# Kernel tuning notes

Measured on AMD Instinct MI355X. Metric: run time of the kernel, lower is better.

Reference implementation:

```python
import jax, jax.numpy as jnp
import numpy as np
from jax import lax

N_RAYS, N_STEPS, G = 4096, 160, 160
COLOR_DIM, WIDTH = 3, 128
POS_PE, VIEW_PE = 5, 4
XYZ_MIN, XYZ_MAX = -1.0, 1.0
NEAR = 0.05
STEPSIZE = 0.5
VOXEL_SIZE = (XYZ_MAX - XYZ_MIN) / G
DIST = STEPSIZE * VOXEL_SIZE
S_VAL = 80.0
FASTCOLOR_THRES = 1e-7
MASK_THRES = 1e-3
ALPHA_INIT = 1e-4
ACT_SHIFT = float(np.log(1.0 / (1.0 - ALPHA_INIT) - 1.0))
SMOOTH_K, SMOOTH_SIGMA = 5, 1.0
POSFREQ = jnp.asarray([2.0 ** i for i in range(POS_PE)], jnp.float32)
VIEWFREQ = jnp.asarray([2.0 ** i for i in range(VIEW_PE)], jnp.float32)


def _gauss_kernel():
    ax = np.arange(SMOOTH_K) - SMOOTH_K // 2
    g = np.exp(-(ax ** 2) / (2.0 * SMOOTH_SIGMA ** 2))
    k = g[:, None, None] * g[None, :, None] * g[None, None, :]
    return jnp.asarray(k / k.sum(), np.float32)[None, None]


def _trilerp(grid, pts):
    # grid [C,Gx,Gx,Gx]; pts [...,3] in world coords -> [..., C] (align_corners trilinear)
    Gx = grid.shape[-1]
    u = (pts - XYZ_MIN) / (XYZ_MAX - XYZ_MIN) * (Gx - 1)
    u = jnp.clip(u, 0.0, Gx - 1.0)
    i0 = jnp.clip(jnp.floor(u).astype(jnp.int32), 0, Gx - 2)
    f = u - i0.astype(u.dtype)
    x0, y0, z0 = i0[..., 0], i0[..., 1], i0[..., 2]
    fx, fy, fz = f[..., 0], f[..., 1], f[..., 2]
    def g8(ix, iy, iz):
        return grid[:, ix, iy, iz]  # [C, ...]
    out = (g8(x0, y0, z0) * (1 - fx) * (1 - fy) * (1 - fz)
         + g8(x0, y0, z0 + 1) * (1 - fx) * (1 - fy) * fz
         + g8(x0, y0 + 1, z0) * (1 - fx) * fy * (1 - fz)
         + g8(x0, y0 + 1, z0 + 1) * (1 - fx) * fy * fz
         + g8(x0 + 1, y0, z0) * fx * (1 - fy) * (1 - fz)
         + g8(x0 + 1, y0, z0 + 1) * fx * (1 - fy) * fz
         + g8(x0 + 1, y0 + 1, z0) * fx * fy * (1 - fz)
         + g8(x0 + 1, y0 + 1, z0 + 1) * fx * fy * fz)
    return jnp.moveaxis(out, 0, -1)


def _alphas2weights(alpha):
    # per-ray (segmented) exclusive cumprod of transmittance; alpha [N,S]
    T = jnp.cumprod(1.0 - alpha, axis=1)
    T_excl = jnp.concatenate([jnp.ones_like(T[:, :1]), T[:, :-1]], axis=1)
    return alpha * T_excl, T[:, -1]


def _mlp(x, w0, b0, w1, b1, w2, b2):
    h = jax.nn.relu(x @ w0 + b0)
    h = jax.nn.relu(h @ w1 + b1)
    return h @ w2 + b2


def _forward(rays_o, rays_d, viewdirs, sdf_grid, mask_density,
             off_color_grid, emo_color_grid,
             off_w0, off_b0, off_w1, off_b1, off_w2, off_b2,
             emo_w0, emo_b0, emo_w1, emo_b1, emo_w2, emo_b2, em_modes):
    N = rays_o.shape[0]
    t = NEAR + DIST * jnp.arange(N_STEPS, dtype=jnp.float32)
    ray_pts = rays_o[:, None, :] + rays_d[:, None, :] * t[None, :, None]  # [N,S,3]

    # MaskCache: threshold alpha from coarse density grid (boolean keep mask)
    dens = _trilerp(mask_density, ray_pts)[..., 0]
    mask_alpha = 1.0 - jnp.exp(-jax.nn.softplus(dens + ACT_SHIFT) * DIST)
    keep0 = mask_alpha >= MASK_THRES  # [N,S]

    # Gaussian-smoothed SDF grid + central-difference gradient grid
    sdf_s = lax.conv_general_dilated(sdf_grid, _gauss_kernel(), (1, 1, 1), 'SAME',
                                     dimension_numbers=('NCDHW', 'OIDHW', 'NCDHW'))[0]  # [1,G,G,G]
    s = sdf_s[0]
    grad_grid = jnp.zeros((3, G, G, G), sdf_grid.dtype)
    grad_grid = grad_grid.at[0, 1:-1].set((s[2:] - s[:-2]) / (2 * VOXEL_SIZE))
    grad_grid = grad_grid.at[1, :, 1:-1].set((s[:, 2:] - s[:, :-2]) / (2 * VOXEL_SIZE))
    grad_grid = grad_grid.at[2, :, :, 1:-1].set((s[:, :, 2:] - s[:, :, :-2]) / (2 * VOXEL_SIZE))

    sdf = _trilerp(sdf_s, ray_pts)[..., 0]   # [N,S]
    gradient = _trilerp(grad_grid, ray_pts)  # [N,S,3]

    # NeuS alpha from sdf (scatter, grad variant, cos_anneal = 1)
    true_cos = jnp.einsum('nd,nsd->ns', viewdirs, gradient)
    iter_cos = -jax.nn.relu(-true_cos)
    prev_cdf = jax.nn.sigmoid((sdf - iter_cos * DIST * 0.5) * S_VAL)
    next_cdf = jax.nn.sigmoid((sdf + iter_cos * DIST * 0.5) * S_VAL)
    alpha = jnp.clip((prev_cdf - next_cdf + 1e-5) / (prev_cdf + 1e-5), 0.0, 1.0)
    alpha = jnp.where(keep0, alpha, 0.0)  # masked points contribute nothing

    weights, _ = _alphas2weights(alpha)
    keep1 = weights > FASTCOLOR_THRES
    alpha = jnp.where(keep1, alpha, 0.0)
    weights, alphainv_last = _alphas2weights(alpha)

    # features: pos PE, view PE (per-ray, gathered by ray_id == broadcast), normal
    rays_xyz = (ray_pts - XYZ_MIN) / (XYZ_MAX - XYZ_MIN)  # [N,S,3]
    xyz_emb = (rays_xyz[..., None] * POSFREQ).reshape(N, N_STEPS, -1)
    v_emb = (viewdirs[..., None] * VIEWFREQ).reshape(N, -1)
    v_full = jnp.concatenate([v_emb, jnp.sin(v_emb), jnp.cos(v_emb)], -1)
    v_full = jnp.broadcast_to(v_full[:, None, :], (N, N_STEPS, v_full.shape[-1]))
    normal = gradient / (jnp.linalg.norm(gradient, axis=-1, keepdims=True) + 1e-5)
    rgb_feat = jnp.concatenate([rays_xyz, jnp.sin(xyz_emb), jnp.cos(xyz_emb), v_full, normal], -1)

    off_in = jnp.concatenate([_trilerp(off_color_grid, ray_pts), rgb_feat], -1)
    emo_in = jnp.concatenate([_trilerp(emo_color_grid, ray_pts), rgb_feat], -1)
    off_rgb = jax.nn.sigmoid(_mlp(off_in, off_w0, off_b0, off_w1, off_b1, off_w2, off_b2))
    emo_rgb = jax.nn.sigmoid(_mlp(emo_in, emo_w0, emo_b0, emo_w1, emo_b1, emo_w2, emo_b2))
    on_mask = (em_modes == 1)[:, None, None]  # em_modes[ray_id] == 1
    rgb = jnp.where(on_mask, emo_rgb, 0.0) + off_rgb

    w_ = weights[..., None]
    rgb_marched = jnp.sum(w_ * rgb, axis=1)  # segment_coo(sum over ray_id)
    cum_weights = jnp.sum(w_, axis=1)        # [N,1]
    return rgb_marched, alphainv_last, 1.0 - cum_weights


def setup_inputs() -> dict:
    key = jax.random.key(0)
    ks = jax.random.split(key, 12)
    rays_o = jax.random.uniform(ks[0], (N_RAYS, 3), jnp.float32, -0.3, 0.3)
    rd = jax.random.normal(ks[1], (N_RAYS, 3), jnp.float32)
    rays_d = rd / jnp.linalg.norm(rd, axis=-1, keepdims=True)
    viewdirs = rays_d
    em_modes = jax.random.randint(ks[2], (N_RAYS,), 0, 2)
    lin = np.linspace(-1.0, 1.0, G, dtype=np.float32)
    x, y, z = np.meshgrid(lin, lin, lin, indexing='ij')
    sdf_grid = jnp.asarray(np.sqrt(x ** 2 + y ** 2 + z ** 2) - 1.0)[None, None]  # sphere-SDF init
    mask_density = jax.random.normal(ks[3], (1, 80, 80, 80), jnp.float32) * 2.0 + 12.0
    off_color_grid = jax.random.normal(ks[4], (COLOR_DIM, G, G, G), jnp.float32) * 0.1
    emo_color_grid = jax.random.normal(ks[5], (COLOR_DIM, G, G, G), jnp.float32) * 0.1
    DIM0 = 3 + 3 * POS_PE * 2 + 3 * VIEW_PE * 3 + COLOR_DIM + 3  # = 75
    def lw(k, i, o):
        return jax.random.normal(k, (i, o), jnp.float32) * (1.0 / np.sqrt(i))
    return dict(rays_o=rays_o, rays_d=rays_d, viewdirs=viewdirs, em_modes=em_modes,
                sdf_grid=sdf_grid, mask_density=mask_density,
                off_color_grid=off_color_grid, emo_color_grid=emo_color_grid,
                off_w0=lw(ks[6], DIM0, WIDTH), off_b0=jnp.zeros((WIDTH,), jnp.float32),
                off_w1=lw(ks[7], WIDTH, WIDTH), off_b1=jnp.zeros((WIDTH,), jnp.float32),
                off_w2=lw(ks[8], WIDTH, 3), off_b2=jnp.zeros((3,), jnp.float32),
                emo_w0=lw(ks[9], DIM0, WIDTH), emo_b0=jnp.zeros((WIDTH,), jnp.float32),
                emo_w1=lw(ks[10], WIDTH, WIDTH), emo_b1=jnp.zeros((WIDTH,), jnp.float32),
                emo_w2=lw(ks[11], WIDTH, 3), emo_b2=jnp.zeros((3,), jnp.float32))


def reference(rays_o, rays_d, viewdirs, em_modes, sdf_grid, mask_density,
              off_color_grid, emo_color_grid,
              off_w0, off_b0, off_w1, off_b1, off_w2, off_b2,
              emo_w0, emo_b0, emo_w1, emo_b1, emo_w2, emo_b2):
    return _forward(rays_o, rays_d, viewdirs, sdf_grid, mask_density,
                    off_color_grid, emo_color_grid,
                    off_w0, off_b0, off_w1, off_b1, off_w2, off_b2,
                    emo_w0, emo_b0, emo_w1, emo_b1, emo_w2, emo_b2, em_modes)
```

## Files before the change

### kernel.cpp

```cpp
#include <hip/hip_runtime.h>

#define NRAYS 4096
#define NSTEPS 160
#define NSAMP (NRAYS*NSTEPS)
#define GG 160
#define GG2 (GG*GG)
#define GG3 (GG*GG2)
#define GM 80
#define GM2 (GM*GM)

#define NEARV 0.05f
#define DISTV 0.00625f
#define SVAL 80.0f
#define ACT_SHIFT_C (-9.2102403669758813f)
#define INV2H 40.0f
#define MASK_THRES_C 1e-3f
#define FAST_THRES_C 1e-7f

#define KW0 0.05448868454964295f
#define KW1 0.24420134200323332f
#define KW2 0.40261994689424750f

__device__ __forceinline__ float sigmf(float x){ return 1.0f/(1.0f+__expf(-x)); }
__device__ __forceinline__ float softplusf_(float x){ return (x>20.0f)? x : log1pf(__expf(x)); }

__device__ __forceinline__ void tricoord(float p, int Gx, int& i0, float& fr){
  float u = (p + 1.0f)*0.5f*(float)(Gx-1);
  u = fminf(fmaxf(u, 0.0f), (float)(Gx-1));
  int i = (int)floorf(u);
  i = min(max(i,0), Gx-2);
  i0 = i; fr = u - (float)i;
}

__global__ __launch_bounds__(256) void ksmooth_yz(const float* __restrict__ in, float* __restrict__ out,
                                                  float* __restrict__ outbuf, int* __restrict__ cnt){
  __shared__ float S[36][37];
  __shared__ float Tz[36][33];
  const int bx = blockIdx.x;
  const int t = threadIdx.x;
  if (bx == 0){
    for (int i = t; i < NRAYS*3; i += 256) outbuf[i] = 0.0f;
    if (t == 0) *cnt = 0;
  }
  const int x  = bx / 25;
  const int tile = bx % 25;
  const int Y0 = (tile/5)*32, Z0 = (tile%5)*32;
  const float kw[5] = {KW0,KW1,KW2,KW1,KW0};
  for (int i = t; i < 36*36; i += 256){
    int r = i/36, c = i - (i/36)*36;
    int y = Y0 + r - 2, z = Z0 + c - 2;
    float v = 0.0f;
    if (y>=0 && y<GG && z>=0 && z<GG) v = in[(x*GG+y)*GG+z];
    S[r][c] = v;
  }
  __syncthreads();
  for (int i = t; i < 36*32; i += 256){
    int r = i >> 5, c = i & 31;
    float acc = 0.f;
    #pragma unroll
    for (int d=0; d<5; d++) acc += kw[d]*S[r][c+d];
    Tz[r][c] = acc;
  }
  __syncthreads();
  for (int i = t; i < 32*32; i += 256){
    int yy = i >> 5, c = i & 31;
    float acc = 0.f;
    #pragma unroll
    for (int d=0; d<5; d++) acc += kw[d]*Tz[yy+d][c];
    out[(x*GG + Y0+yy)*GG + Z0 + c] = acc;
  }
}

__global__ __launch_bounds__(64) void kmarch(
  const float* __restrict__ ro, const float* __restrict__ rd,
  const float* __restrict__ vd, const float* __restrict__ maskg,
  const float* __restrict__ Y,
  int* __restrict__ slist, float* __restrict__ sw, float* __restrict__ sgrad,
  int* __restrict__ cnt, float* __restrict__ out)
{
  int n = blockIdx.x*64 + threadIdx.x;
  if (n >= NRAYS) return;
  const float ox=ro[n*3+0], oy=ro[n*3+1], oz=ro[n*3+2];
  const float dx=rd[n*3+0], dy=rd[n*3+1], dz=rd[n*3+2];
  const float vx=vd[n*3+0], vy=vd[n*3+1], vz=vd[n*3+2];
  const float kwc[5] = {KW0,KW1,KW2,KW1,KW0};
  float T1=1.0f, T2=1.0f, cum=0.0f;
  for (int s=0; s<NSTEPS; s++){
    float tt = NEARV + DISTV*(float)s;
    float px = ox + dx*tt, py = oy + dy*tt, pz = oz + dz*tt;

    int mx,my,mz; float mfx,mfy,mfz;
    tricoord(px, GM, mx, mfx); tricoord(py, GM, my, mfy); tricoord(pz, GM, mz, mfz);
    int mid = (mx*GM + my)*GM + mz;
    float d000=maskg[mid],        d001=maskg[mid+1];
    float d010=maskg[mid+GM],     d011=maskg[mid+GM+1];
    float d100=maskg[mid+GM2],    d101=maskg[mid+GM2+1];
    float d110=maskg[mid+GM2+GM], d111=maskg[mid+GM2+GM+1];
    float m00 = d000 + (d001-d000)*mfz;
    float m01 = d010 + (d011-d010)*mfz;
    float m10 = d100 + (d101-d100)*mfz;
    float m11 = d110 + (d111-d110)*mfz;
    float m0 = m00 + (m01-m00)*mfy;
    float m1 = m10 + (m11-m10)*mfy;
    float dens = m0 + (m1-m0)*mfx;
    float malpha = 1.0f - __expf(-softplusf_(dens + ACT_SHIFT_C)*DISTV);

    int ix,iy,iz; float fx,fy,fz;
    tricoord(px, GG, ix, fx); tricoord(py, GG, iy, fy); tricoord(pz, GG, iz, fz);

    float R[2][2][8];
    #pragma unroll
    for (int jb=0;jb<2;jb++)
      #pragma unroll
      for (int jc=0;jc<2;jc++)
        #pragma unroll
        for (int j=0;j<8;j++){
          int a = ix-3+j;
          R[jb][jc][j] = (a>=0 && a<GG) ? Y[(a*GG + iy+jb)*GG + iz+jc] : 0.0f;
        }
    const bool hasym = (iy>=1), hasyp = (iy<=GG-3);
    const bool haszm = (iz>=1), haszp = (iz<=GG-3);
    float Eym[2][6], Eyp[2][6], Ezm[2][6], Ezp[2][6];
    #pragma unroll
    for (int jc=0;jc<2;jc++)
      #pragma unroll
      for (int j=0;j<6;j++){
        int a = ix-2+j;
        bool ax = (a>=0 && a<GG);
        Eym[jc][j] = (hasym && ax) ? Y[(a*GG + iy-1)*GG + iz+jc] : 0.0f;
        Eyp[jc][j] = (hasyp && ax) ? Y[(a*GG + iy+2)*GG + iz+jc] : 0.0f;
      }
    #pragma unroll
    for (int jb=0;jb<2;jb++)
      #pragma unroll
      for (int j=0;j<6;j++){
        int a = ix-2+j;
        bool ax = (a>=0 && a<GG);
        Ezm[jb][j] = (haszm && ax) ? Y[(a*GG + iy+jb)*GG + iz-1] : 0.0f;
        Ezp[jb][j] = (haszp && ax) ? Y[(a*GG + iy+jb)*GG + iz+2] : 0.0f;
      }

    float sdf=0.0f, gx=0.0f, gy=0.0f, gz=0.0f;
    #pragma unroll
    for (int ja=0;ja<2;ja++){
      #pragma unroll
      for (int jb=0;jb<2;jb++){
        #pragma unroll
        for (int jc=0;jc<2;jc++){
          float w = (ja?fx:1.0f-fx)*(jb?fy:1.0f-fy)*(jc?fz:1.0f-fz);
          const float* r = R[jb][jc];
          float s0=0.0f;
          #pragma unroll
          for (int t2=0;t2<5;t2++) s0 += kwc[t2]*r[ja+1+t2];
          sdf += w*s0;
          int a = ix+ja, b = iy+jb, c = iz+jc;
          if (a>=1 && a<=GG-2){
            float sp=0.0f, sm=0.0f;
            #pragma unroll
            for (int t2=0;t2<5;t2++){ sp += kwc[t2]*r[ja+2+t2]; sm += kwc[t2]*r[ja+t2]; }
            gx += w*INV2H*(sp-sm);
          }
          if (b>=1 && b<=GG-2){
            float acc=0.0f;
            if (jb==0){
              const float* up = R[1][jc];
              const float* dn = Eym[jc];
              #pragma unroll
              for (int t2=0;t2<5;t2++) acc += kwc[t2]*(up[ja+1+t2] - dn[ja+t2]);
            } else {
              const float* up = Eyp[jc];
              const float* dn = R[0][jc];
              #pragma unroll
              for (int t2=0;t2<5;t2++) acc += kwc[t2]*(up[ja+t2] - dn[ja+1+t2]);
            }
            gy += w*INV2H*acc;
          }
          if (c>=1 && c<=GG-2){
            float acc=0.0f;
            if (jc==0){
              const float* up = R[jb][1];
              const float* dn = Ezm[jb];
              #pragma unroll
              for (int t2=0;t2<5;t2++) acc += kwc[t2]*(up[ja+1+t2] - dn[ja+t2]);
            } else {
              const float* up = Ezp[jb];
              const float* dn = R[jb][0];
              #pragma unroll
              for (int t2=0;t2<5;t2++) acc += kwc[t2]*(up[ja+t2] - dn[ja+1+t2]);
            }
            gz += w*INV2H*acc;
          }
        }
      }
    }

    float tc = vx*gx + vy*gy + vz*gz;
    float icos = fminf(tc, 0.0f);
    float e = icos*DISTV*0.5f;
    float prev = sigmf((sdf - e)*SVAL);
    float nxt  = sigmf((sdf + e)*SVAL);
    float alpha = (prev - nxt + 1e-5f)/(prev + 1e-5f);
    alpha = fminf(fmaxf(alpha, 0.0f), 1.0f);
    if (!(malpha >= MASK_THRES_C)) alpha = 0.0f;

    float w1 = alpha*T1; T1 *= (1.0f - alpha);
    float a2 = (w1 > FAST_THRES_C) ? alpha : 0.0f;
    float wv = a2*T2;   T2 *= (1.0f - a2);
    cum += wv;
    if (wv > 0.0f){
      int pos = atomicAdd(cnt, 1);
      slist[pos] = n*NSTEPS + s;
      sw[pos] = wv;
      sgrad[pos*3+0]=gx; sgrad[pos*3+1]=gy; sgrad[pos*3+2]=gz;
    }
    if (T1 <= FAST_THRES_C) break;
  }
  out[NRAYS*3 + n] = T2;
  out[NRAYS*4 + n] = 1.0f - cum;
}

__global__ __launch_bounds__(256) void kmlp3(
  const float* __restrict__ ro, const float* __restrict__ rd,
  const float* __restrict__ vd, const int* __restrict__ em,
  const float* __restrict__ offc, const float* __restrict__ emoc,
  const int* __restrict__ slist, const float* __restrict__ sw,
  const float* __restrict__ sgrad, const int* __restrict__ cnt,
  const float* __restrict__ W0o, const float* __restrict__ b0o,
  const float* __restrict__ W1o, const float* __restrict__ b1o,
  const float* __restrict__ W2o, const float* __restrict__ b2o,
  const float* __restrict__ W0e, const float* __restrict__ b0e,
  const float* __restrict__ W1e, const float* __restrict__ b1e,
  const float* __restrict__ W2e, const float* __restrict__ b2e,
  float* __restrict__ out)
{
  __shared__ float X[8][80];
  __shared__ float H[8][132];
  __shared__ float H2[8][132];
  __shared__ float OUTB[8][3];
  __shared__ float WSH[8];
  __shared__ float GS[8][3];
  __shared__ int SSAMP[8];
  __shared__ int SEM[8];
  __shared__ int s_go;

  const int t = threadIdx.x;
  const int count = *cnt;
  const int head = blockIdx.x & 1;
  const int cstride = gridDim.x >> 1;

  const float* W0 = head ? W0e : W0o;  const float* b0 = head ? b0e : b0o;
  const float* W1 = head ? W1e : W1o;  const float* b1 = head ? b1e : b1o;
  const float* W2 = head ? W2e : W2o;  const float* b2 = head ? b2e : b2o;
  const float* cg = head ? emoc : offc;
  const float4* W04 = (const float4*)W0;
  const float4* W14 = (const float4*)W1;

  const int sp   = t >> 5;
  const int lane = t & 31;

  for (int chunk = blockIdx.x >> 1; chunk*8 < count; chunk += cstride) {
    const int base = chunk*8;
    if (t == 0) s_go = 0;
    if (t < 8) {
      int i = base + t;
      bool vld = (i < count);
      int samp = vld ? slist[i] : 0;
      SSAMP[t] = samp;
      WSH[t]   = vld ? sw[i] : 0.0f;
      GS[t][0] = vld ? sgrad[i*3+0] : 0.0f;
      GS[t][1] = vld ? sgrad[i*3+1] : 0.0f;
      GS[t][2] = vld ? sgrad[i*3+2] : 0.0f;
      SEM[t]   = vld ? em[samp/NSTEPS] : 0;
    }
    __syncthreads();
    if (t < 8) {
      bool live = (WSH[t] > 0.0f) && (head == 0 || SEM[t] != 0);
      if (live) s_go = 1;
    }
    __syncthreads();

    if (s_go) {
      {
        const int s = t & 7;
        const int r = t >> 3;
        const int samp = SSAMP[s];
        const int n = samp / NSTEPS;
        const int step = samp - n*NSTEPS;
        const float tt = NEARV + DISTV*(float)step;
        const float px = ro[n*3+0] + rd[n*3+0]*tt;
        const float py = ro[n*3+1] + rd[n*3+1]*tt;
        const float pz = ro[n*3+2] + rd[n*3+2]*tt;
        if (r < 3) {
          int ix,iy,iz; float fx,fy,fz;
          tricoord(px, GG, ix, fx); tricoord(py, GG, iy, fy); tricoord(pz, GG, iz, fz);
          const float* g = cg + (size_t)r * GG3;
          const int id = (ix*GG + iy)*GG + iz;
          float v000=g[id],        v001=g[id+1];
          float v010=g[id+GG],     v011=g[id+GG+1];
          float v100=g[id+GG2],    v101=g[id+GG2+1];
          float v110=g[id+GG2+GG], v111=g[id+GG2+GG+1];
          float c00 = v000 + (v001-v000)*fz;
          float c01 = v010 + (v011-v010)*fz;
          float c10 = v100 + (v101-v100)*fz;
          float c11 = v110 + (v111-v110)*fz;
          float c0 = c00 + (c01-c00)*fy;
          float c1 = c10 + (c11-c10)*fy;
          X[s][r] = c0 + (c1-c0)*fx;
        } else if (r == 3) {
          X[s][3] = (px+1.0f)*0.5f;
          X[s][4] = (py+1.0f)*0.5f;
          X[s][5] = (pz+1.0f)*0.5f;
          float gx = GS[s][0], gy = GS[s][1], gz = GS[s][2];
          float inv = 1.0f/(sqrtf(gx*gx+gy*gy+gz*gz)+1e-5f);
          X[s][72] = gx*inv; X[s][73] = gy*inv; X[s][74] = gz*inv;
        } else if (r < 7) {
          const int a = r - 4;
          const float coord = (a==0)?px:((a==1)?py:pz);
          const float rxyz = (coord+1.0f)*0.5f;
          float fr = 1.0f;
          #pragma unroll
          for (int q = 0; q < 5; q++) {
            float e = rxyz*fr; fr *= 2.0f;
            X[s][6  + a*5 + q] = __sinf(e);
            X[s][21 + a*5 + q] = __cosf(e);
          }
        } else if (r < 10) {
          const int a = r - 7;
          const float v = vd[n*3+a];
          float fr = 1.0f;
          #pragma unroll
          for (int q = 0; q < 4; q++) {
            float e = v*fr; fr *= 2.0f;
            X[s][36 + a*4 + q] = e;
            X[s][48 + a*4 + q] = __sinf(e);
            X[s][60 + a*4 + q] = __cosf(e);
          }
        }
      }
      __syncthreads();

      {
        float4 acc = ((const float4*)b0)[lane];
        #pragma unroll 5
        for (int k=0; k<75; k++){
          float x = X[sp][k];
          float4 w = W04[k*32 + lane];
          acc.x += x*w.x; acc.y += x*w.y; acc.z += x*w.z; acc.w += x*w.w;
        }
        H[sp][lane*4+0] = fmaxf(acc.x,0.0f);
        H[sp][lane*4+1] = fmaxf(acc.y,0.0f);
        H[sp][lane*4+2] = fmaxf(acc.z,0.0f);
        H[sp][lane*4+3] = fmaxf(acc.w,0.0f);
      }
      __syncthreads();

      {
        float4 acc = ((const float4*)b1)[lane];
        #pragma unroll 8
        for (int k=0; k<128; k++){
          float x = H[sp][k];
          float4 w = W14[k*32 + lane];
          acc.x += x*w.x; acc.y += x*w.y; acc.z += x*w.z; acc.w += x*w.w;
        }
        H2[sp][lane*4+0] = fmaxf(acc.x,0.0f);
        H2[sp][lane*4+1] = fmaxf(acc.y,0.0f);
        H2[sp][lane*4+2] = fmaxf(acc.z,0.0f);
        H2[sp][lane*4+3] = fmaxf(acc.w,0.0f);
      }
      __syncthreads();

      {
        float a0=0.0f, a1=0.0f, a2v=0.0f;
        #pragma unroll
        for (int i=0;i<4;i++){
          int k = lane*4+i;
          float h = H2[sp][k];
          a0  += h*W2[k*3+0];
          a1  += h*W2[k*3+1];
          a2v += h*W2[k*3+2];
        }
        #pragma unroll
        for (int d=16; d>=1; d>>=1){
          a0  += __shfl_down(a0,  d, 32);
          a1  += __shfl_down(a1,  d, 32);
          a2v += __shfl_down(a2v, d, 32);
        }
        if (lane == 0){
          OUTB[sp][0] = sigmf(a0  + b2[0]);
          OUTB[sp][1] = sigmf(a1  + b2[1]);
          OUTB[sp][2] = sigmf(a2v + b2[2]);
        }
      }
      __syncthreads();

      if (t < 24) {
        int s2 = t/3, c = t - s2*3;
        float w = WSH[s2];
        if (w > 0.0f && (head == 0 || SEM[s2] != 0)) {
          int n2 = SSAMP[s2]/NSTEPS;
          atomicAdd(&out[n2*3 + c], w * OUTB[s2][c]);
        }
      }
    }
    __syncthreads();
  }
}

extern "C" void kernel_launch(void* const* d_in, const int* in_sizes, int n_in,
                              void* d_out, int out_size, void* d_ws, size_t ws_size,
                              hipStream_t stream) {
  const float* ro    = (const float*)d_in[0];
  const float* rd    = (const float*)d_in[1];
  const float* vd    = (const float*)d_in[2];
  const int*   em    = (const int*)d_in[3];
  const float* sdfg  = (const float*)d_in[4];
  const float* maskg = (const float*)d_in[5];
  const float* offc  = (const float*)d_in[6];
  const float* emoc  = (const float*)d_in[7];
  const float* W0o = (const float*)d_in[8];
  const float* b0o = (const float*)d_in[9];
  const float* W1o = (const float*)d_in[10];
  const float* b1o = (const float*)d_in[11];
  const float* W2o = (const float*)d_in[12];
  const float* b2o = (const float*)d_in[13];
  const float* W0e = (const float*)d_in[14];
  const float* b0e = (const float*)d_in[15];
  const float* W1e = (const float*)d_in[16];
  const float* b1e = (const float*)d_in[17];
  const float* W2e = (const float*)d_in[18];
  const float* b2e = (const float*)d_in[19];

  float* out = (float*)d_out;
  float* ws  = (float*)d_ws;
  float* bufB  = ws;
  float* swb   = ws + GG3;
  float* sgradb= swb + NSAMP;
  int*   slist = (int*)(sgradb + 3*(size_t)NSAMP);
  int*   cnt   = slist + NSAMP;

  ksmooth_yz<<<GG*25, 256, 0, stream>>>(sdfg, bufB, out, cnt);

  kmarch<<<NRAYS/64, 64, 0, stream>>>(ro, rd, vd, maskg, bufB,
                                      slist, swb, sgradb, cnt, out);

  kmlp3<<<2048, 256, 0, stream>>>(ro, rd, vd, em, offc, emoc,
                                  slist, swb, sgradb, cnt,
                                  W0o,b0o,W1o,b1o,W2o,b2o,
                                  W0e,b0e,W1e,b1e,W2e,b2e, out);
}
```

Measured before the change: 66.89 us.

## Register-block MLP over four samples per warp with 32-sample chunks

The MLP kernel now handles 32 samples per block instead of 8. Each 32-lane group computes four samples at once, so every weight float4 loaded from global memory is reused across four accumulators, and inputs are read from shared memory as float4. Feature-building work is spread over the 8 thread rows, with view encoding merged into the positional-encoding threads, and the grid is cut to 512 blocks. This is meant to cut the weight load traffic per sample, at the cost of more registers, more shared memory and fewer blocks to spread the work.

```diff
diff --git a/kernel.cpp b/kernel.cpp
--- a/kernel.cpp
+++ b/kernel.cpp
@@ -219,7 +219,7 @@
   out[NRAYS*4 + n] = 1.0f - cum;
 }
 
-__global__ __launch_bounds__(256) void kmlp3(
+__global__ __launch_bounds__(256) void kmlp5(
   const float* __restrict__ ro, const float* __restrict__ rd,
   const float* __restrict__ vd, const int* __restrict__ em,
   const float* __restrict__ offc, const float* __restrict__ emoc,
@@ -233,14 +233,14 @@
   const float* __restrict__ W2e, const float* __restrict__ b2e,
   float* __restrict__ out)
 {
-  __shared__ float X[8][80];
-  __shared__ float H[8][132];
-  __shared__ float H2[8][132];
-  __shared__ float OUTB[8][3];
-  __shared__ float WSH[8];
-  __shared__ float GS[8][3];
-  __shared__ int SSAMP[8];
-  __shared__ int SEM[8];
+  __shared__ float X[32][80];
+  __shared__ float H[32][132];
+  __shared__ float H2[32][132];
+  __shared__ float OUTB[32][3];
+  __shared__ float WSH[32];
+  __shared__ float GS[32][3];
+  __shared__ int SSAMP[32];
+  __shared__ int SEM[32];
   __shared__ int s_go;
 
   const int t = threadIdx.x;
@@ -255,13 +255,13 @@
   const float4* W04 = (const float4*)W0;
   const float4* W14 = (const float4*)W1;
 
-  const int sp   = t >> 5;
   const int lane = t & 31;
-
-  for (int chunk = blockIdx.x >> 1; chunk*8 < count; chunk += cstride) {
-    const int base = chunk*8;
+  const int sg   = t >> 5;
+
+  for (int chunk = blockIdx.x >> 1; chunk*32 < count; chunk += cstride) {
+    const int base = chunk*32;
     if (t == 0) s_go = 0;
-    if (t < 8) {
+    if (t < 32) {
       int i = base + t;
       bool vld = (i < count);
       int samp = vld ? slist[i] : 0;
@@ -273,7 +273,7 @@
       SEM[t]   = vld ? em[samp/NSTEPS] : 0;
     }
     __syncthreads();
-    if (t < 8) {
+    if (t < 32) {
       bool live = (WSH[t] > 0.0f) && (head == 0 || SEM[t] != 0);
       if (live) s_go = 1;
     }
@@ -281,8 +281,8 @@
 
     if (s_go) {
       {
-        const int s = t & 7;
-        const int r = t >> 3;
+        const int s = t & 31;
+        const int r = t >> 5;
         const int samp = SSAMP[s];
         const int n = samp / NSTEPS;
         const int step = samp - n*NSTEPS;
@@ -313,6 +313,7 @@
           float gx = GS[s][0], gy = GS[s][1], gz = GS[s][2];
           float inv = 1.0f/(sqrtf(gx*gx+gy*gy+gz*gz)+1e-5f);
           X[s][72] = gx*inv; X[s][73] = gy*inv; X[s][74] = gz*inv;
+          X[s][75] = 0.0f; X[s][76] = 0.0f; X[s][77] = 0.0f; X[s][78] = 0.0f; X[s][79] = 0.0f;
         } else if (r < 7) {
           const int a = r - 4;
           const float coord = (a==0)?px:((a==1)?py:pz);
@@ -324,13 +325,11 @@
             X[s][6  + a*5 + q] = __sinf(e);
             X[s][21 + a*5 + q] = __cosf(e);
           }
-        } else if (r < 10) {
-          const int a = r - 7;
           const float v = vd[n*3+a];
-          float fr = 1.0f;
+          float fr2 = 1.0f;
           #pragma unroll
           for (int q = 0; q < 4; q++) {
-            float e = v*fr; fr *= 2.0f;
+            float e = v*fr2; fr2 *= 2.0f;
             X[s][36 + a*4 + q] = e;
             X[s][48 + a*4 + q] = __sinf(e);
             X[s][60 + a*4 + q] = __cosf(e);
@@ -340,60 +339,126 @@
       __syncthreads();
 
       {
-        float4 acc = ((const float4*)b0)[lane];
-        #pragma unroll 5
-        for (int k=0; k<75; k++){
-          float x = X[sp][k];
+        const float4 bb = ((const float4*)b0)[lane];
+        float4 a0 = bb, a1 = bb, a2 = bb, a3 = bb;
+        const int s0 = sg*4;
+        #pragma unroll 2
+        for (int k4 = 0; k4 < 72; k4 += 4){
+          float4 w0 = W04[(k4+0)*32 + lane];
+          float4 w1 = W04[(k4+1)*32 + lane];
+          float4 w2 = W04[(k4+2)*32 + lane];
+          float4 w3 = W04[(k4+3)*32 + lane];
+          float4 x0 = *(const float4*)&X[s0+0][k4];
+          float4 x1 = *(const float4*)&X[s0+1][k4];
+          float4 x2 = *(const float4*)&X[s0+2][k4];
+          float4 x3 = *(const float4*)&X[s0+3][k4];
+          a0.x+=x0.x*w0.x; a0.y+=x0.x*w0.y; a0.z+=x0.x*w0.z; a0.w+=x0.x*w0.w;
+          a1.x+=x1.x*w0.x; a1.y+=x1.x*w0.y; a1.z+=x1.x*w0.z; a1.w+=x1.x*w0.w;
+          a2.x+=x2.x*w0.x; a2.y+=x2.x*w0.y; a2.z+=x2.x*w0.z; a2.w+=x2.x*w0.w;
+          a3.x+=x3.x*w0.x; a3.y+=x3.x*w0.y; a3.z+=x3.x*w0.z; a3.w+=x3.x*w0.w;
+          a0.x+=x0.y*w1.x; a0.y+=x0.y*w1.y; a0.z+=x0.y*w1.z; a0.w+=x0.y*w1.w;
+          a1.x+=x1.y*w1.x; a1.y+=x1.y*w1.y; a1.z+=x1.y*w1.z; a1.w+=x1.y*w1.w;
+          a2.x+=x2.y*w1.x; a2.y+=x2.y*w1.y; a2.z+=x2.y*w1.z; a2.w+=x2.y*w1.w;
+          a3.x+=x3.y*w1.x; a3.y+=x3.y*w1.y; a3.z+=x3.y*w1.z; a3.w+=x3.y*w1.w;
+          a0.x+=x0.z*w2.x; a0.y+=x0.z*w2.y; a0.z+=x0.z*w2.z; a0.w+=x0.z*w2.w;
+          a1.x+=x1.z*w2.x; a1.y+=x1.z*w2.y; a1.z+=x1.z*w2.z; a1.w+=x1.z*w2.w;
+          a2.x+=x2.z*w2.x; a2.y+=x2.z*w2.y; a2.z+=x2.z*w2.z; a2.w+=x2.z*w2.w;
+          a3.x+=x3.z*w2.x; a3.y+=x3.z*w2.y; a3.z+=x3.z*w2.z; a3.w+=x3.z*w2.w;
+          a0.x+=x0.w*w3.x; a0.y+=x0.w*w3.y; a0.z+=x0.w*w3.z; a0.w+=x0.w*w3.w;
+          a1.x+=x1.w*w3.x; a1.y+=x1.w*w3.y; a1.z+=x1.w*w3.z; a1.w+=x1.w*w3.w;
+          a2.x+=x2.w*w3.x; a2.y+=x2.w*w3.y; a2.z+=x2.w*w3.z; a2.w+=x2.w*w3.w;
+          a3.x+=x3.w*w3.x; a3.y+=x3.w*w3.y; a3.z+=x3.w*w3.z; a3.w+=x3.w*w3.w;
+        }
+        #pragma unroll
+        for (int k = 72; k < 75; k++){
           float4 w = W04[k*32 + lane];
-          acc.x += x*w.x; acc.y += x*w.y; acc.z += x*w.z; acc.w += x*w.w;
-        }
-        H[sp][lane*4+0] = fmaxf(acc.x,0.0f);
-        H[sp][lane*4+1] = fmaxf(acc.y,0.0f);
-        H[sp][lane*4+2] = fmaxf(acc.z,0.0f);
-        H[sp][lane*4+3] = fmaxf(acc.w,0.0f);
+          float x0 = X[s0+0][k], x1 = X[s0+1][k], x2 = X[s0+2][k], x3 = X[s0+3][k];
+          a0.x+=x0*w.x; a0.y+=x0*w.y; a0.z+=x0*w.z; a0.w+=x0*w.w;
+          a1.x+=x1*w.x; a1.y+=x1*w.y; a1.z+=x1*w.z; a1.w+=x1*w.w;
+          a2.x+=x2*w.x; a2.y+=x2*w.y; a2.z+=x2*w.z; a2.w+=x2*w.w;
+          a3.x+=x3*w.x; a3.y+=x3*w.y; a3.z+=x3*w.z; a3.w+=x3*w.w;
+        }
+        H[s0+0][lane*4+0]=fmaxf(a0.x,0.f); H[s0+0][lane*4+1]=fmaxf(a0.y,0.f);
+        H[s0+0][lane*4+2]=fmaxf(a0.z,0.f); H[s0+0][lane*4+3]=fmaxf(a0.w,0.f);
+        H[s0+1][lane*4+0]=fmaxf(a1.x,0.f); H[s0+1][lane*4+1]=fmaxf(a1.y,0.f);
+        H[s0+1][lane*4+2]=fmaxf(a1.z,0.f); H[s0+1][lane*4+3]=fmaxf(a1.w,0.f);
+        H[s0+2][lane*4+0]=fmaxf(a2.x,0.f); H[s0+2][lane*4+1]=fmaxf(a2.y,0.f);
+        H[s0+2][lane*4+2]=fmaxf(a2.z,0.f); H[s0+2][lane*4+3]=fmaxf(a2.w,0.f);
+        H[s0+3][lane*4+0]=fmaxf(a3.x,0.f); H[s0+3][lane*4+1]=fmaxf(a3.y,0.f);
+        H[s0+3][lane*4+2]=fmaxf(a3.z,0.f); H[s0+3][lane*4+3]=fmaxf(a3.w,0.f);
       }
       __syncthreads();
 
       {
-        float4 acc = ((const float4*)b1)[lane];
-        #pragma unroll 8
-        for (int k=0; k<128; k++){
-          float x = H[sp][k];
-          float4 w = W14[k*32 + lane];
-          acc.x += x*w.x; acc.y += x*w.y; acc.z += x*w.z; acc.w += x*w.w;
-        }
-        H2[sp][lane*4+0] = fmaxf(acc.x,0.0f);
-        H2[sp][lane*4+1] = fmaxf(acc.y,0.0f);
-        H2[sp][lane*4+2] = fmaxf(acc.z,0.0f);
-        H2[sp][lane*4+3] = fmaxf(acc.w,0.0f);
+        const float4 bb = ((const float4*)b1)[lane];
+        float4 a0 = bb, a1 = bb, a2 = bb, a3 = bb;
+        const int s0 = sg*4;
+        #pragma unroll 2
+        for (int k4 = 0; k4 < 128; k4 += 4){
+          float4 w0 = W14[(k4+0)*32 + lane];
+          float4 w1 = W14[(k4+1)*32 + lane];
+          float4 w2 = W14[(k4+2)*32 + lane];
+          float4 w3 = W14[(k4+3)*32 + lane];
+          float4 x0 = *(const float4*)&H[s0+0][k4];
+          float4 x1 = *(const float4*)&H[s0+1][k4];
+          float4 x2 = *(const float4*)&H[s0+2][k4];
+          float4 x3 = *(const float4*)&H[s0+3][k4];
+          a0.x+=x0.x*w0.x; a0.y+=x0.x*w0.y; a0.z+=x0.x*w0.z; a0.w+=x0.x*w0.w;
+          a1.x+=x1.x*w0.x; a1.y+=x1.x*w0.y; a1.z+=x1.x*w0.z; a1.w+=x1.x*w0.w;
+          a2.x+=x2.x*w0.x; a2.y+=x2.x*w0.y; a2.z+=x2.x*w0.z; a2.w+=x2.x*w0.w;
+          a3.x+=x3.x*w0.x; a3.y+=x3.x*w0.y; a3.z+=x3.x*w0.z; a3.w+=x3.x*w0.w;
+          a0.x+=x0.y*w1.x; a0.y+=x0.y*w1.y; a0.z+=x0.y*w1.z; a0.w+=x0.y*w1.w;
+          a1.x+=x1.y*w1.x; a1.y+=x1.y*w1.y; a1.z+=x1.y*w1.z; a1.w+=x1.y*w1.w;
+          a2.x+=x2.y*w1.x; a2.y+=x2.y*w1.y; a2.z+=x2.y*w1.z; a2.w+=x2.y*w1.w;
+          a3.x+=x3.y*w1.x; a3.y+=x3.y*w1.y; a3.z+=x3.y*w1.z; a3.w+=x3.y*w1.w;
+          a0.x+=x0.z*w2.x; a0.y+=x0.z*w2.y; a0.z+=x0.z*w2.z; a0.w+=x0.z*w2.w;
+          a1.x+=x1.z*w2.x; a1.y+=x1.z*w2.y; a1.z+=x1.z*w2.z; a1.w+=x1.z*w2.w;
+          a2.x+=x2.z*w2.x; a2.y+=x2.z*w2.y; a2.z+=x2.z*w2.z; a2.w+=x2.z*w2.w;
+          a3.x+=x3.z*w2.x; a3.y+=x3.z*w2.y; a3.z+=x3.z*w2.z; a3.w+=x3.z*w2.w;
+          a0.x+=x0.w*w3.x; a0.y+=x0.w*w3.y; a0.z+=x0.w*w3.z; a0.w+=x0.w*w3.w;
+          a1.x+=x1.w*w3.x; a1.y+=x1.w*w3.y; a1.z+=x1.w*w3.z; a1.w+=x1.w*w3.w;
+          a2.x+=x2.w*w3.x; a2.y+=x2.w*w3.y; a2.z+=x2.w*w3.z; a2.w+=x2.w*w3.w;
+          a3.x+=x3.w*w3.x; a3.y+=x3.w*w3.y; a3.z+=x3.w*w3.z; a3.w+=x3.w*w3.w;
+        }
+        H2[s0+0][lane*4+0]=fmaxf(a0.x,0.f); H2[s0+0][lane*4+1]=fmaxf(a0.y,0.f);
+        H2[s0+0][lane*4+2]=fmaxf(a0.z,0.f); H2[s0+0][lane*4+3]=fmaxf(a0.w,0.f);
+        H2[s0+1][lane*4+0]=fmaxf(a1.x,0.f); H2[s0+1][lane*4+1]=fmaxf(a1.y,0.f);
+        H2[s0+1][lane*4+2]=fmaxf(a1.z,0.f); H2[s0+1][lane*4+3]=fmaxf(a1.w,0.f);
+        H2[s0+2][lane*4+0]=fmaxf(a2.x,0.f); H2[s0+2][lane*4+1]=fmaxf(a2.y,0.f);
+        H2[s0+2][lane*4+2]=fmaxf(a2.z,0.f); H2[s0+2][lane*4+3]=fmaxf(a2.w,0.f);
+        H2[s0+3][lane*4+0]=fmaxf(a3.x,0.f); H2[s0+3][lane*4+1]=fmaxf(a3.y,0.f);
+        H2[s0+3][lane*4+2]=fmaxf(a3.z,0.f); H2[s0+3][lane*4+3]=fmaxf(a3.w,0.f);
       }
       __syncthreads();
 
       {
-        float a0=0.0f, a1=0.0f, a2v=0.0f;
+        const int s0 = sg*4;
         #pragma unroll
-        for (int i=0;i<4;i++){
-          int k = lane*4+i;
-          float h = H2[sp][k];
-          a0  += h*W2[k*3+0];
-          a1  += h*W2[k*3+1];
-          a2v += h*W2[k*3+2];
-        }
-        #pragma unroll
-        for (int d=16; d>=1; d>>=1){
-          a0  += __shfl_down(a0,  d, 32);
-          a1  += __shfl_down(a1,  d, 32);
-          a2v += __shfl_down(a2v, d, 32);
-        }
-        if (lane == 0){
-          OUTB[sp][0] = sigmf(a0  + b2[0]);
-          OUTB[sp][1] = sigmf(a1  + b2[1]);
-          OUTB[sp][2] = sigmf(a2v + b2[2]);
+        for (int i = 0; i < 4; i++){
+          const int s = s0 + i;
+          float4 h = *(const float4*)&H2[s][lane*4];
+          float c0 = h.x*W2[(lane*4+0)*3+0] + h.y*W2[(lane*4+1)*3+0]
+                   + h.z*W2[(lane*4+2)*3+0] + h.w*W2[(lane*4+3)*3+0];
+          float c1 = h.x*W2[(lane*4+0)*3+1] + h.y*W2[(lane*4+1)*3+1]
+                   + h.z*W2[(lane*4+2)*3+1] + h.w*W2[(lane*4+3)*3+1];
+          float c2 = h.x*W2[(lane*4+0)*3+2] + h.y*W2[(lane*4+1)*3+2]
+                   + h.z*W2[(lane*4+2)*3+2] + h.w*W2[(lane*4+3)*3+2];
+          #pragma unroll
+          for (int d=16; d>=1; d>>=1){
+            c0 += __shfl_down(c0, d, 32);
+            c1 += __shfl_down(c1, d, 32);
+            c2 += __shfl_down(c2, d, 32);
+          }
+          if (lane == 0){
+            OUTB[s][0] = sigmf(c0 + b2[0]);
+            OUTB[s][1] = sigmf(c1 + b2[1]);
+            OUTB[s][2] = sigmf(c2 + b2[2]);
+          }
         }
       }
       __syncthreads();
 
-      if (t < 24) {
+      if (t < 96) {
         int s2 = t/3, c = t - s2*3;
         float w = WSH[s2];
         if (w > 0.0f && (head == 0 || SEM[s2] != 0)) {
@@ -432,19 +497,19 @@
 
   float* out = (float*)d_out;
   float* ws  = (float*)d_ws;
-  float* bufB  = ws;
+  float* Yb    = ws;
   float* swb   = ws + GG3;
   float* sgradb= swb + NSAMP;
   int*   slist = (int*)(sgradb + 3*(size_t)NSAMP);
   int*   cnt   = slist + NSAMP;
 
-  ksmooth_yz<<<GG*25, 256, 0, stream>>>(sdfg, bufB, out, cnt);
-
-  kmarch<<<NRAYS/64, 64, 0, stream>>>(ro, rd, vd, maskg, bufB,
+  ksmooth_yz<<<GG*25, 256, 0, stream>>>(sdfg, Yb, out, cnt);
+
+  kmarch<<<NRAYS/64, 64, 0, stream>>>(ro, rd, vd, maskg, Yb,
                                       slist, swb, sgradb, cnt, out);
 
-  kmlp3<<<2048, 256, 0, stream>>>(ro, rd, vd, em, offc, emoc,
-                                  slist, swb, sgradb, cnt,
-                                  W0o,b0o,W1o,b1o,W2o,b2o,
-                                  W0e,b0e,W1e,b1e,W2e,b2e, out);
+  kmlp5<<<512, 256, 0, stream>>>(ro, rd, vd, em, offc, emoc,
+                                 slist, swb, sgradb, cnt,
+                                 W0o,b0o,W1o,b1o,W2o,b2o,
+                                 W0e,b0e,W1e,b1e,W2e,b2e, out);
 }
```

Result: faster. 54.29 us (-18.8%).
